# Optimization experiments

Measured on AMD Instinct MI355X. Metric: run time of the kernel, lower is better.

Reference implementation:

```python
import jax, jax.numpy as jnp
import numpy as np

B, S, C, H, D = 4, 1024, 1024, 16, 64
MAX_POS = 512
SPAN = min(max(S, S), MAX_POS)  # rel_attn_span = 512
SCALE = 1.0 / np.sqrt(3.0 * D)


def setup_inputs() -> dict:
    key = jax.random.key(0)
    ks = jax.random.split(key, 10)
    std = 0.02
    return {
        "hidden_states": jax.random.normal(ks[0], (B, S, C), jnp.float32),
        "rel_embeddings": jax.random.normal(ks[1], (2 * MAX_POS, C), jnp.float32),
        "Wq": jax.random.normal(ks[2], (C, H, D), jnp.float32) * std,
        "bq": jnp.zeros((H, D), jnp.float32),
        "Wk": jax.random.normal(ks[3], (C, H, D), jnp.float32) * std,
        "Wv": jax.random.normal(ks[4], (C, H, D), jnp.float32) * std,
        "bv": jnp.zeros((H, D), jnp.float32),
        "Wc2p": jax.random.normal(ks[5], (C, H, D), jnp.float32) * std,
        "Wp2c": jax.random.normal(ks[6], (C, H, D), jnp.float32) * std,
        "bp2c": jnp.zeros((H, D), jnp.float32),
        "Wo": jax.random.normal(ks[7], (C, C), jnp.float32) * std,
        "bo": jnp.zeros((C,), jnp.float32),
    }


def reference(hidden_states, rel_embeddings, Wq, bq, Wk, Wv, bv, Wc2p, Wp2c, bp2c, Wo, bo):
    # Projections: 'abc,cde->abde'  -> [B,S,H,D]
    q = jnp.einsum("bsc,chd->bshd", hidden_states, Wq) + bq
    k = jnp.einsum("bsc,chd->bshd", hidden_states, Wk)
    v = jnp.einsum("bsc,chd->bshd", hidden_states, Wv) + bv

    q = q * SCALE
    # content-to-content scores: 'aecd,abcd->acbe' -> [B,H,Q,K]
    scores = jnp.einsum("bkhd,bqhd->bhqk", k, q)

    # relative-position ids: rel_pos[q,k] = q - k, shape [S,S]
    ids = jnp.arange(S, dtype=jnp.int32)
    rel_pos = ids[:, None] - ids[None, :]

    # slice rel table to the active span (full table here since S >= MAX_POS)
    rel = rel_embeddings[MAX_POS - SPAN : MAX_POS + SPAN, :]  # [2*SPAN, C]

    # c2p: pos_key [2*SPAN,H,D]; scores [B,H,Q,2*SPAN]; gather along last axis
    pos_key = jnp.einsum("rc,chd->rhd", rel, Wc2p)
    c2p = jnp.einsum("bqhd,rhd->bhqr", q, pos_key)
    c2p_pos = jnp.clip(rel_pos + SPAN, 0, 2 * SPAN - 1)  # [Q,K]
    c2p_idx = jnp.broadcast_to(c2p_pos[None, None], (B, H, S, S))
    c2p_g = jnp.take_along_axis(c2p, c2p_idx, axis=-1)

    # p2c: pos_query (scaled) [2*SPAN,H,D]; scores [B,H,K,2*SPAN]
    pos_query = (jnp.einsum("rc,chd->rhd", rel, Wp2c) + bp2c) * SCALE
    p2c = jnp.einsum("bkhd,rhd->bhkr", k, pos_query)
    p2c_pos = jnp.clip(-rel_pos + SPAN, 0, 2 * SPAN - 1)  # [K,K]
    p2c_idx = jnp.broadcast_to(p2c_pos[None, None], (B, H, S, S))
    p2c_g = jnp.take_along_axis(p2c, p2c_idx, axis=-1)

    scores = scores + c2p_g + p2c_g
    # NOTE: source calls _masked_softmax without passing attention_mask -> plain softmax
    probs = jax.nn.softmax(scores, axis=-1)

    # 'acbe,aecd->abcd' -> [B,Q,H,D]
    attn_out = jnp.einsum("bhqk,bkhd->bqhd", probs, v)
    attn_out = attn_out.reshape(B, S, H * D)
    return jnp.einsum("bsc,cd->bsd", attn_out, Wo) + bo
```

## Files before the change

### kernel.cpp

```cpp
#include <hip/hip_runtime.h>
#include <cmath>

#define SCALE_F 0.07216878364870322f

typedef unsigned short u16;
typedef __attribute__((ext_vector_type(8))) __bf16 bf16x8;
typedef __attribute__((ext_vector_type(4))) float f32x4;
typedef __attribute__((ext_vector_type(16))) float f32x16;

#define MFMA16(a, b, c) __builtin_amdgcn_mfma_f32_16x16x32_bf16(a, b, c, 0, 0, 0)
#define MFMA32(a, b, c) __builtin_amdgcn_mfma_f32_32x32x16_bf16(a, b, c, 0, 0, 0)

__device__ __forceinline__ u16 f2bf(float x) {
    unsigned u = __float_as_uint(x);
    unsigned r = (u + 0x7fffu + ((u >> 16) & 1u)) >> 16;
    return (u16)r;
}
__device__ __forceinline__ float bf2f(u16 u) {
    return __uint_as_float(((unsigned)u) << 16);
}
__device__ __forceinline__ void split2(float x, u16& h, u16& l) {
    h = f2bf(x);
    l = f2bf(x - bf2f(h));
}

__device__ __forceinline__ void glds16(const u16* g, u16* s) {
    __builtin_amdgcn_global_load_lds(
        (const __attribute__((address_space(1))) unsigned int*)g,
        (__attribute__((address_space(3))) unsigned int*)s,
        16, 0, 0);
}

__device__ __forceinline__ bf16x8 frg(const u16* base, int row, int ch) {
    return *(const bf16x8*)(base + (row << 6) + ((ch ^ (row & 7)) << 3));
}

__global__ __launch_bounds__(256) void split_rows2(
    const float* __restrict__ x0, u16* __restrict__ h0, u16* __restrict__ l0,
    int nblk0,
    const float* __restrict__ x1, u16* __restrict__ h1, u16* __restrict__ l1)
{
    const float* x; u16* h; u16* l; int bx = blockIdx.x;
    if (bx < nblk0) { x = x0; h = h0; l = l0; }
    else { x = x1; h = h1; l = l1; bx -= nblk0; }
    int i = (bx * 256 + threadIdx.x) << 2;
    float4 v = *(const float4*)(x + i);
    ushort4 hv, lv;
    split2(v.x, hv.x, lv.x); split2(v.y, hv.y, lv.y);
    split2(v.z, hv.z, lv.z); split2(v.w, hv.w, lv.w);
    *(ushort4*)(h + i) = hv;
    *(ushort4*)(l + i) = lv;
}

__global__ __launch_bounds__(256) void transpose3(
    const float* __restrict__ W0, u16* __restrict__ Th0, u16* __restrict__ Tl0,
    const float* __restrict__ W1, u16* __restrict__ Th1, u16* __restrict__ Tl1,
    const float* __restrict__ W2, u16* __restrict__ Th2, u16* __restrict__ Tl2)
{
    const float* W; u16* Th; u16* Tl;
    if (blockIdx.z == 0)      { W = W0; Th = Th0; Tl = Tl0; }
    else if (blockIdx.z == 1) { W = W1; Th = Th1; Tl = Tl1; }
    else                      { W = W2; Th = Th2; Tl = Tl2; }
    __shared__ float t[64][65];
    const int tid = threadIdx.x;
    const int r = tid >> 4, c4 = (tid & 15) << 2;
    const int k0 = blockIdx.y << 6, n0 = blockIdx.x << 6;
#pragma unroll
    for (int p = 0; p < 4; ++p) {
        int row = (p << 4) + r;
        float4 v = *(const float4*)(W + (size_t)(k0 + row) * 1024 + n0 + c4);
        t[row][c4] = v.x; t[row][c4 + 1] = v.y; t[row][c4 + 2] = v.z; t[row][c4 + 3] = v.w;
    }
    __syncthreads();
#pragma unroll
    for (int p = 0; p < 4; ++p) {
        int nr = (p << 4) + r;
        float a = t[c4 + 0][nr];
        float b = t[c4 + 1][nr];
        float c = t[c4 + 2][nr];
        float d = t[c4 + 3][nr];
        ushort4 hv, lv;
        split2(a, hv.x, lv.x); split2(b, hv.y, lv.y);
        split2(c, hv.z, lv.z); split2(d, hv.w, lv.w);
        *(ushort4*)(Th + (size_t)(n0 + nr) * 1024 + k0 + c4) = hv;
        *(ushort4*)(Tl + (size_t)(n0 + nr) * 1024 + k0 + c4) = lv;
    }
}

struct GD {
    const u16 *Ah, *Al, *Bh, *Bl;
    const float* bias;
    float* Cf;
    u16 *Ch, *Cl;
    int N, K;
    float scale;
    int mode;
};

__global__ __launch_bounds__(256, 2) void gemm_mfma(GD d0, GD d1, int xsplit)
{
    __shared__ u16 sAh[128 * 32];
    __shared__ u16 sAl[128 * 32];
    __shared__ u16 sBh[128 * 32];
    __shared__ u16 sBl[128 * 32];

    const GD d = (blockIdx.x < (unsigned)xsplit) ? d0 : d1;
    const int bx = (blockIdx.x < (unsigned)xsplit) ? blockIdx.x : blockIdx.x - xsplit;
    const int N = d.N, K = d.K;

    const int tid = threadIdx.x;
    const int wv = tid >> 6, lane = tid & 63;
    const int quad = lane >> 4, ln = lane & 15;
    const int wr = wv & 1, wc = wv >> 1;
    const int m0 = blockIdx.y << 7, n0 = bx << 7;

    const u16* gsrc = (wv == 0) ? d.Ah : (wv == 1) ? d.Al : (wv == 2) ? d.Bh : d.Bl;
    u16* sdst = (wv == 0) ? sAh : (wv == 1) ? sAl : (wv == 2) ? sBh : sBl;
    const int row0 = (wv < 2) ? m0 : n0;
    const u16* gbase = gsrc + (size_t)(row0 + (lane >> 2)) * K + ((lane & 3) << 3);

    f32x4 acc[4][4];
#pragma unroll
    for (int f = 0; f < 4; ++f)
#pragma unroll
        for (int g = 0; g < 4; ++g) acc[f][g] = (f32x4){0.f, 0.f, 0.f, 0.f};

    const u16* pa_h = sAh + ((wr << 6) + ln) * 32 + (quad << 3);
    const u16* pa_l = sAl + ((wr << 6) + ln) * 32 + (quad << 3);
    const u16* pb_h = sBh + ((wc << 6) + ln) * 32 + (quad << 3);
    const u16* pb_l = sBl + ((wc << 6) + ln) * 32 + (quad << 3);

#pragma unroll
    for (int t = 0; t < 8; ++t)
        glds16(gbase + (size_t)(t << 4) * K, sdst + t * 512);

    for (int kt = 0; kt < K; kt += 32) {
        __syncthreads();
        bf16x8 bhv[4], blv[4], ahv[4], alv[4];
#pragma unroll
        for (int g = 0; g < 4; ++g) {
            bhv[g] = *(const bf16x8*)(pb_h + g * 512);
            blv[g] = *(const bf16x8*)(pb_l + g * 512);
            ahv[g] = *(const bf16x8*)(pa_h + g * 512);
            alv[g] = *(const bf16x8*)(pa_l + g * 512);
        }
        __syncthreads();
        if (kt + 32 < K) {
#pragma unroll
            for (int t = 0; t < 8; ++t)
                glds16(gbase + (size_t)(t << 4) * K + (kt + 32), sdst + t * 512);
        }
#pragma unroll
        for (int f = 0; f < 4; ++f) {
#pragma unroll
            for (int g = 0; g < 4; ++g) {
                acc[f][g] = MFMA16(ahv[f], bhv[g], acc[f][g]);
                acc[f][g] = MFMA16(ahv[f], blv[g], acc[f][g]);
                acc[f][g] = MFMA16(alv[f], bhv[g], acc[f][g]);
            }
        }
    }

    if (d.mode == 0) {
#pragma unroll
        for (int f = 0; f < 4; ++f) {
            int row = m0 + (wr << 6) + (f << 4) + (quad << 2);
#pragma unroll
            for (int g = 0; g < 4; ++g) {
                int col = n0 + (wc << 6) + (g << 4) + ln;
                float bb = d.bias ? d.bias[col] : 0.f;
#pragma unroll
                for (int r = 0; r < 4; ++r)
                    d.Cf[(size_t)(row + r) * N + col] = (acc[f][g][r] + bb) * d.scale;
            }
        }
    } else if (d.mode == 1) {
#pragma unroll
        for (int f = 0; f < 4; ++f) {
            int row = m0 + (wr << 6) + (f << 4) + (quad << 2);
#pragma unroll
            for (int g = 0; g < 4; ++g) {
                int col = n0 + (wc << 6) + (g << 4) + ln;
                float bb = d.bias ? d.bias[col] : 0.f;
#pragma unroll
                for (int r = 0; r < 4; ++r) {
                    float v = (acc[f][g][r] + bb) * d.scale;
                    u16 hh, ll;
                    split2(v, hh, ll);
                    d.Ch[(size_t)(row + r) * N + col] = hh;
                    d.Cl[(size_t)(row + r) * N + col] = ll;
                }
            }
        }
    } else if (d.mode == 2) {
#pragma unroll
        for (int f = 0; f < 4; ++f) {
            int row = m0 + (wr << 6) + (f << 4) + (quad << 2);
#pragma unroll
            for (int g = 0; g < 4; ++g) {
                int col = n0 + (wc << 6) + (g << 4) + ln;
                size_t obase = (size_t)(col >> 10) * 1048576 + (col & 1023);
#pragma unroll
                for (int r = 0; r < 4; ++r) {
                    float v = acc[f][g][r] + (d.bias ? d.bias[row + r] : 0.f);
                    u16 hh, ll;
                    split2(v, hh, ll);
                    size_t idx = obase + (size_t)(row + r) * 1024;
                    d.Ch[idx] = hh;
                    d.Cl[idx] = ll;
                }
            }
        }
    } else {
#pragma unroll
        for (int f = 0; f < 4; ++f) {
            int row = m0 + (wr << 6) + (f << 4) + (quad << 2);
#pragma unroll
            for (int g = 0; g < 4; ++g) {
                int col = n0 + (wc << 6) + (g << 4) + ln;
                float bb = d.bias ? d.bias[col] : 0.f;
#pragma unroll
                for (int r = 0; r < 4; ++r)
                    d.Ch[(size_t)(row + r) * N + col] =
                        f2bf((acc[f][g][r] + bb) * d.scale);
            }
        }
    }
}

__global__ __launch_bounds__(256, 2) void gemm_mfma_64(GD d0, GD d1, int xsplit)
{
    __shared__ u16 sAh[64 * 32];
    __shared__ u16 sAl[64 * 32];
    __shared__ u16 sBh[128 * 32];
    __shared__ u16 sBl[128 * 32];

    const GD d = (blockIdx.x < (unsigned)xsplit) ? d0 : d1;
    const int bx = (blockIdx.x < (unsigned)xsplit) ? blockIdx.x : blockIdx.x - xsplit;
    const int N = d.N, K = d.K;

    const int tid = threadIdx.x;
    const int wv = tid >> 6, lane = tid & 63;
    const int quad = lane >> 4, ln = lane & 15;
    const int wr = wv & 1, wc = wv >> 1;
    const int m0 = blockIdx.y << 6, n0 = bx << 7;

    const u16* gsrc = (wv == 0) ? d.Ah : (wv == 1) ? d.Al : (wv == 2) ? d.Bh : d.Bl;
    u16* sdst = (wv == 0) ? sAh : (wv == 1) ? sAl : (wv == 2) ? sBh : sBl;
    const int row0 = (wv < 2) ? m0 : n0;
    const int nt = (wv < 2) ? 4 : 8;
    const u16* gbase = gsrc + (size_t)(row0 + (lane >> 2)) * K + ((lane & 3) << 3);

    f32x4 acc[2][4];
#pragma unroll
    for (int f = 0; f < 2; ++f)
#pragma unroll
        for (int g = 0; g < 4; ++g) acc[f][g] = (f32x4){0.f, 0.f, 0.f, 0.f};

    const u16* pa_h = sAh + ((wr << 5) + ln) * 32 + (quad << 3);
    const u16* pa_l = sAl + ((wr << 5) + ln) * 32 + (quad << 3);
    const u16* pb_h = sBh + ((wc << 6) + ln) * 32 + (quad << 3);
    const u16* pb_l = sBl + ((wc << 6) + ln) * 32 + (quad << 3);

#pragma unroll
    for (int t = 0; t < 8; ++t)
        if (t < nt) glds16(gbase + (size_t)(t << 4) * K, sdst + t * 512);

    for (int kt = 0; kt < K; kt += 32) {
        __syncthreads();
        bf16x8 bhv[4], blv[4], ahv[2], alv[2];
#pragma unroll
        for (int g = 0; g < 4; ++g) {
            bhv[g] = *(const bf16x8*)(pb_h + g * 512);
            blv[g] = *(const bf16x8*)(pb_l + g * 512);
        }
#pragma unroll
        for (int f = 0; f < 2; ++f) {
            ahv[f] = *(const bf16x8*)(pa_h + f * 512);
            alv[f] = *(const bf16x8*)(pa_l + f * 512);
        }
        __syncthreads();
        if (kt + 32 < K) {
#pragma unroll
            for (int t = 0; t < 8; ++t)
                if (t < nt)
                    glds16(gbase + (size_t)(t << 4) * K + (kt + 32), sdst + t * 512);
        }
#pragma unroll
        for (int f = 0; f < 2; ++f) {
#pragma unroll
            for (int g = 0; g < 4; ++g) {
                acc[f][g] = MFMA16(ahv[f], bhv[g], acc[f][g]);
                acc[f][g] = MFMA16(ahv[f], blv[g], acc[f][g]);
                acc[f][g] = MFMA16(alv[f], bhv[g], acc[f][g]);
            }
        }
    }

    if (d.mode == 0) {
#pragma unroll
        for (int f = 0; f < 2; ++f) {
            int row = m0 + (wr << 5) + (f << 4) + (quad << 2);
#pragma unroll
            for (int g = 0; g < 4; ++g) {
                int col = n0 + (wc << 6) + (g << 4) + ln;
                float bb = d.bias ? d.bias[col] : 0.f;
#pragma unroll
                for (int r = 0; r < 4; ++r)
                    d.Cf[(size_t)(row + r) * N + col] = (acc[f][g][r] + bb) * d.scale;
            }
        }
    } else if (d.mode == 2) {
#pragma unroll
        for (int f = 0; f < 2; ++f) {
            int row = m0 + (wr << 5) + (f << 4) + (quad << 2);
#pragma unroll
            for (int g = 0; g < 4; ++g) {
                int col = n0 + (wc << 6) + (g << 4) + ln;
                size_t obase = (size_t)(col >> 10) * 1048576 + (col & 1023);
#pragma unroll
                for (int r = 0; r < 4; ++r) {
                    float v = acc[f][g][r] + (d.bias ? d.bias[row + r] : 0.f);
                    u16 hh, ll;
                    split2(v, hh, ll);
                    size_t idx = obase + (size_t)(row + r) * 1024;
                    d.Ch[idx] = hh;
                    d.Cl[idx] = ll;
                }
            }
        }
    } else if (d.mode == 3) {
#pragma unroll
        for (int f = 0; f < 2; ++f) {
            int row = m0 + (wr << 5) + (f << 4) + (quad << 2);
#pragma unroll
            for (int g = 0; g < 4; ++g) {
                int col = n0 + (wc << 6) + (g << 4) + ln;
                float bb = d.bias ? d.bias[col] : 0.f;
#pragma unroll
                for (int r = 0; r < 4; ++r)
                    d.Ch[(size_t)(row + r) * N + col] =
                        f2bf((acc[f][g][r] + bb) * d.scale);
            }
        }
    } else {
#pragma unroll
        for (int f = 0; f < 2; ++f) {
            int row = m0 + (wr << 5) + (f << 4) + (quad << 2);
#pragma unroll
            for (int g = 0; g < 4; ++g) {
                int col = n0 + (wc << 6) + (g << 4) + ln;
                float bb = d.bias ? d.bias[col] : 0.f;
#pragma unroll
                for (int r = 0; r < 4; ++r) {
                    float v = (acc[f][g][r] + bb) * d.scale;
                    u16 hh, ll;
                    split2(v, hh, ll);
                    d.Ch[(size_t)(row + r) * N + col] = hh;
                    d.Cl[(size_t)(row + r) * N + col] = ll;
                }
            }
        }
    }
}

__global__ __launch_bounds__(256, 2) void attn_mfma(
    const u16* Qh_g, const u16* Ql_g,
    const u16* __restrict__ Kh_g, const u16* __restrict__ Kl_g,
    const u16* __restrict__ VTh_g, const u16* __restrict__ VTl_g,
    const u16* __restrict__ PKh_g, const u16* __restrict__ PQh_g,
    u16* outh, u16* outl)
{
    __shared__ __align__(16) unsigned char smem[67840];
    u16* Kh_s  = (u16*)smem;
    u16* Kl_s  = (u16*)(smem + 8192);
    u16* PKs   = (u16*)(smem + 16384);
    u16* VTh_s = (u16*)(smem + 16384);
    u16* VTl_s = (u16*)(smem + 24576);
    u16* PQs   = (u16*)(smem + 32768);
    u16* Ph    = (u16*)(smem + 49152);
    u16* Pl    = (u16*)(smem + 58368);
    float* Mbase = (float*)(smem + 49152);
    float* l_s = (float*)(smem + 67584);

    const int tid = threadIdx.x;
    const int wv = tid >> 6, lane = tid & 63;
    const int half = lane >> 5, lc = lane & 31;
    const int rw = wv & 1, cw = wv >> 1;
    const int b = blockIdx.z, h = blockIdx.y;
    const int q0 = blockIdx.x << 6, hd0 = h << 6;
    float* Mw = Mbase + wv * 1056;

    const int rloc = lane >> 3;
    const int k4e  = (((lane & 7) ^ rloc) << 3);

    bf16x8 qfh[4], qfl[4], kfh[4], kfl[4];
    const size_t arow = ((size_t)(b * 1024 + q0 + (rw << 5) + lc) << 10) + hd0 + (half << 3);
    {
#pragma unroll
        for (int c = 0; c < 4; ++c) {
            qfh[c] = *(const bf16x8*)(Qh_g + arow + (c << 4));
            qfl[c] = *(const bf16x8*)(Ql_g + arow + (c << 4));
            kfh[c] = *(const bf16x8*)(Kh_g + arow + (c << 4));
            kfl[c] = *(const bf16x8*)(Kl_g + arow + (c << 4));
        }
    }
    if (tid < 64) l_s[tid] = 0.f;

    f32x16 o;
    float l_part[16];
#pragma unroll
    for (int r = 0; r < 16; ++r) { o[r] = 0.f; l_part[r] = 0.f; }

    const int sbC = (rw - cw + 1) << 5;
    const int sbP = (cw - rw + 1) << 5;

    {
#pragma unroll
        for (int t = 0; t < 2; ++t) {
            int call = wv + (t << 2);
            int row = (call << 3) + rloc;
            size_t g = ((size_t)(b * 1024 + 0 + row) << 10) + hd0 + k4e;
            glds16(Kh_g + g, Kh_s + (call << 9));
            glds16(Kl_g + g, Kl_s + (call << 9));
        }
        const int baseC = q0 + 449, baseP = -q0 + 449;
#pragma unroll
        for (int t = 0; t < 4; ++t) {
            int call = wv + (t << 2);
            int row = (call << 3) + rloc;
            int rc = min(max(baseC + row, 0), 1023);
            int rp = min(max(baseP + row, 0), 1023);
            glds16(PKh_g + (((size_t)rc << 10) + hd0 + k4e), PKs + (call << 9));
            glds16(PQh_g + (((size_t)rp << 10) + hd0 + k4e), PQs + (call << 9));
        }
    }
    __syncthreads();

    for (int kt = 0; kt < 16; ++kt) {
        const int k0 = kt << 6;
        f32x16 s;
#pragma unroll
        for (int r = 0; r < 16; ++r) s[r] = 0.f;
        {
            const int krow = (cw << 5) + lc;
#pragma unroll
            for (int c = 0; c < 4; ++c) {
                int ch = (c << 1) + half;
                bf16x8 bh = frg(Kh_s, krow, ch);
                bf16x8 bl = frg(Kl_s, krow, ch);
                s = MFMA32(qfh[c], bh, s);
                s = MFMA32(qfh[c], bl, s);
                s = MFMA32(qfl[c], bh, s);
            }
        }
        {
            f32x16 M0, M1;
#pragma unroll
            for (int r = 0; r < 16; ++r) { M0[r] = 0.f; M1[r] = 0.f; }
#pragma unroll
            for (int c = 0; c < 4; ++c) {
                int ch = (c << 1) + half;
                bf16x8 b0 = frg(PKs, sbC + lc, ch);
                bf16x8 b1 = frg(PKs, sbC + 32 + lc, ch);
                M0 = MFMA32(qfh[c], b0, M0); M0 = MFMA32(qfl[c], b0, M0);
                M1 = MFMA32(qfh[c], b1, M1); M1 = MFMA32(qfl[c], b1, M1);
            }
#pragma unroll
            for (int r = 0; r < 16; ++r) {
                int m = (r & 3) + ((r >> 2) << 3) + (half << 2);
                bool u = (lc >= m);
                float val = u ? M0[r] : M1[r];
                int nn = m - lc + (u ? 31 : -1);
                Mw[m * 33 + nn] = val;
            }
#pragma unroll
            for (int r = 0; r < 16; ++r) {
                int m = (r & 3) + ((r >> 2) << 3) + (half << 2);
                s[r] += Mw[m * 33 + lc];
            }
        }
        {
            f32x16 M0, M1;
#pragma unroll
            for (int r = 0; r < 16; ++r) { M0[r] = 0.f; M1[r] = 0.f; }
#pragma unroll
            for (int c = 0; c < 4; ++c) {
                int ch = (c << 1) + half;
                bf16x8 b0 = frg(PQs, sbP + lc, ch);
                bf16x8 b1 = frg(PQs, sbP + 32 + lc, ch);
                M0 = MFMA32(kfh[c], b0, M0); M0 = MFMA32(kfl[c], b0, M0);
                M1 = MFMA32(kfh[c], b1, M1); M1 = MFMA32(kfl[c], b1, M1);
            }
#pragma unroll
            for (int r = 0; r < 16; ++r) {
                int m = (r & 3) + ((r >> 2) << 3) + (half << 2);
                bool u = (lc >= 31 - m);
                float val = u ? M0[r] : M1[r];
                int nn = lc + m + (u ? -31 : 1);
                Mw[m * 33 + nn] = val;
            }
#pragma unroll
            for (int r = 0; r < 16; ++r) {
                int m = (r & 3) + ((r >> 2) << 3) + (half << 2);
                s[r] += Mw[m * 33 + lc];
            }
        }
#pragma unroll
        for (int r = 0; r < 16; ++r) {
            s[r] = __expf(s[r]);
            l_part[r] += s[r];
        }
        __syncthreads();
        {
#pragma unroll
            for (int t = 0; t < 2; ++t) {
                int call = wv + (t << 2);
                int row = (call << 3) + rloc;
                size_t g = ((size_t)((b * 16 + h) * 64 + row) << 10) + k0 + k4e;
                glds16(VTh_g + g, VTh_s + (call << 9));
                glds16(VTl_g + g, VTl_s + (call << 9));
            }
        }
#pragma unroll
        for (int r = 0; r < 16; ++r) {
            int m = (r & 3) + ((r >> 2) << 3) + (half << 2);
            int addr = ((rw << 5) + m) * 72 + (cw << 5) + lc;
            u16 hh, ll;
            split2(s[r], hh, ll);
            Ph[addr] = hh;
            Pl[addr] = ll;
        }
        __syncthreads();
        {
            const u16* ap  = Ph + ((rw << 5) + lc) * 72 + (half << 3);
            const u16* apl = Pl + ((rw << 5) + lc) * 72 + (half << 3);
            const int vrow = (cw << 5) + lc;
#pragma unroll
            for (int c = 0; c < 4; ++c) {
                int ch = (c << 1) + half;
                bf16x8 ah = *(const bf16x8*)(ap + (c << 4));
                bf16x8 al = *(const bf16x8*)(apl + (c << 4));
                bf16x8 bh = frg(VTh_s, vrow, ch);
                bf16x8 bl = frg(VTl_s, vrow, ch);
                o = MFMA32(ah, bh, o);
                o = MFMA32(ah, bl, o);
                o = MFMA32(al, bh, o);
            }
        }
        __syncthreads();
        {
            const int k0n = ((kt + 1) & 15) << 6;
#pragma unroll
            for (int t = 0; t < 2; ++t) {
                int call = wv + (t << 2);
                int row = (call << 3) + rloc;
                size_t g = ((size_t)(b * 1024 + k0n + row) << 10) + hd0 + k4e;
                glds16(Kh_g + g, Kh_s + (call << 9));
                glds16(Kl_g + g, Kl_s + (call << 9));
            }
            const int baseC = q0 - k0n + 449, baseP = k0n - q0 + 449;
#pragma unroll
            for (int t = 0; t < 4; ++t) {
                int call = wv + (t << 2);
                int row = (call << 3) + rloc;
                int rc = min(max(baseC + row, 0), 1023);
                int rp = min(max(baseP + row, 0), 1023);
                glds16(PKh_g + (((size_t)rc << 10) + hd0 + k4e), PKs + (call << 9));
                glds16(PQh_g + (((size_t)rp << 10) + hd0 + k4e), PQs + (call << 9));
            }
        }
        __syncthreads();
    }
#pragma unroll
    for (int r = 0; r < 16; ++r) {
        float v = l_part[r];
#pragma unroll
        for (int off = 1; off < 32; off <<= 1) v += __shfl_xor(v, off, 64);
        int m = (r & 3) + ((r >> 2) << 3) + (half << 2);
        if (lc == 0) atomicAdd(&l_s[(rw << 5) + m], v);
    }
    __syncthreads();
#pragma unroll
    for (int r = 0; r < 16; ++r) {
        int m = (r & 3) + ((r >> 2) << 3) + (half << 2);
        int row = (rw << 5) + m;
        float inv = 1.f / l_s[row];
        size_t g = ((size_t)(b * 1024 + q0 + row) << 10) + hd0 + (cw << 5) + lc;
        u16 hh, ll;
        split2(o[r] * inv, hh, ll);
        outh[g] = hh;
        outl[g] = ll;
    }
}

extern "C" void kernel_launch(void* const* d_in, const int* in_sizes, int n_in,
                              void* d_out, int out_size, void* d_ws, size_t ws_size,
                              hipStream_t stream)
{
    (void)in_sizes; (void)n_in; (void)out_size; (void)ws_size;
    const float* hidden = (const float*)d_in[0];
    const float* rel    = (const float*)d_in[1];
    const float* Wq   = (const float*)d_in[2];
    const float* bq   = (const float*)d_in[3];
    const float* Wk   = (const float*)d_in[4];
    const float* Wv   = (const float*)d_in[5];
    const float* bv   = (const float*)d_in[6];
    const float* Wc2p = (const float*)d_in[7];
    const float* Wp2c = (const float*)d_in[8];
    const float* bp2c = (const float*)d_in[9];
    const float* Wo   = (const float*)d_in[10];
    const float* bo   = (const float*)d_in[11];
    float* out = (float*)d_out;

    u16* U = (u16*)d_ws;
    const size_t MU = 1048576;
    u16* Hh  = U;              u16* Hl  = U + 4 * MU;
    u16* Rh  = U + 8 * MU;     u16* Rl  = U + 9 * MU;
    u16* WtAh = U + 10 * MU;   u16* WtAl = U + 11 * MU;
    u16* Qh  = U + 12 * MU;    u16* Ql  = U + 16 * MU;
    u16* Kh  = U + 20 * MU;    u16* Kl  = U + 24 * MU;
    u16* VTh = U + 28 * MU;    u16* VTl = U + 32 * MU;
    u16* WkTh = U + 28 * MU;   u16* WkTl = U + 29 * MU;
    u16* PKh = U + 0 * MU;
    u16* PQh = U + 2 * MU;
    u16* Wp2cTh = U + 4 * MU;  u16* Wp2cTl = U + 5 * MU;
    u16* WoTh = U + 6 * MU;    u16* WoTl = U + 7 * MU;

    dim3 blk(256);

    hipLaunchKernelGGL(split_rows2, dim3(5120), blk, 0, stream,
                       hidden, Hh, Hl, 4096, rel, Rh, Rl);

    hipLaunchKernelGGL(transpose3, dim3(16, 16, 2), blk, 0, stream,
                       Wq, WtAh, WtAl, Wk, WkTh, WkTl,
                       (const float*)nullptr, (u16*)nullptr, (u16*)nullptr);

    {
        GD dQ = {Hh, Hl, WtAh, WtAl, bq, nullptr, Qh, Ql, 1024, 1024, SCALE_F, 1};
        GD dK = {Hh, Hl, WkTh, WkTl, nullptr, nullptr, Kh, Kl, 1024, 1024, 1.f, 1};
        hipLaunchKernelGGL(gemm_mfma, dim3(16, 32), blk, 0, stream, dQ, dK, 8);
    }

    hipLaunchKernelGGL(transpose3, dim3(16, 16, 1), blk, 0, stream,
                       Wv, WtAh, WtAl,
                       (const float*)nullptr, (u16*)nullptr, (u16*)nullptr,
                       (const float*)nullptr, (u16*)nullptr, (u16*)nullptr);

    {
        GD dV = {WtAh, WtAl, Hh, Hl, bv, nullptr, VTh, VTl, 4096, 1024, 1.f, 2};
        hipLaunchKernelGGL(gemm_mfma_64, dim3(32, 16), blk, 0, stream, dV, dV, 9999);
    }

    hipLaunchKernelGGL(transpose3, dim3(16, 16, 3), blk, 0, stream,
                       Wc2p, WtAh, WtAl, Wp2c, Wp2cTh, Wp2cTl, Wo, WoTh, WoTl);

    {
        GD dPK = {Rh, Rl, WtAh, WtAl, nullptr, nullptr, PKh, nullptr, 1024, 1024, 1.f, 3};
        GD dPQ = {Rh, Rl, Wp2cTh, Wp2cTl, bp2c, nullptr, PQh, nullptr, 1024, 1024, SCALE_F, 3};
        hipLaunchKernelGGL(gemm_mfma_64, dim3(16, 16), blk, 0, stream, dPK, dPQ, 8);
    }

    hipLaunchKernelGGL(attn_mfma, dim3(16, 16, 4), blk, 0, stream,
                       Qh, Ql, Kh, Kl, VTh, VTl, PKh, PQh, Qh, Ql);

    {
        GD dO = {Qh, Ql, WoTh, WoTl, bo, out, nullptr, nullptr, 1024, 1024, 1.f, 0};
        hipLaunchKernelGGL(gemm_mfma_64, dim3(8, 64), blk, 0, stream, dO, dO, 9999);
    }
}
```

Before: 468.0 us.

## Double-buffer GEMM LDS tiles and restructure attention loop to overlap V loads

Both GEMM kernels now hold two LDS stages. The load for the next K-tile is issued right after the barrier into the alternate buffer, which removes one of the two barriers per iteration. In the attention kernel, V^T and P get their own LDS regions, so the V^T tile load starts at the top of each KV iteration and overlaps the score computation. The P·V MFMAs are moved after the next K/PK/PQ prefetch, and the P buffer uses an XOR-swizzled layout read through the same fragment helper. This doubles LDS per block (GEMM 64KB, attention 80KB), which can lower occupancy relative to the launch_bounds(256,2) target.

```diff
diff --git a/kernel.cpp b/kernel.cpp
--- a/kernel.cpp
+++ b/kernel.cpp
@@ -99,10 +99,10 @@
 
 __global__ __launch_bounds__(256, 2) void gemm_mfma(GD d0, GD d1, int xsplit)
 {
-    __shared__ u16 sAh[128 * 32];
-    __shared__ u16 sAl[128 * 32];
-    __shared__ u16 sBh[128 * 32];
-    __shared__ u16 sBl[128 * 32];
+    __shared__ u16 sAh[8192];
+    __shared__ u16 sAl[8192];
+    __shared__ u16 sBh[8192];
+    __shared__ u16 sBl[8192];
 
     const GD d = (blockIdx.x < (unsigned)xsplit) ? d0 : d1;
     const int bx = (blockIdx.x < (unsigned)xsplit) ? blockIdx.x : blockIdx.x - xsplit;
@@ -134,21 +134,23 @@
     for (int t = 0; t < 8; ++t)
         glds16(gbase + (size_t)(t << 4) * K, sdst + t * 512);
 
+    int cur = 0;
     for (int kt = 0; kt < K; kt += 32) {
         __syncthreads();
+        if (kt + 32 < K) {
+            u16* nd = sdst + ((cur ^ 1) << 12);
+#pragma unroll
+            for (int t = 0; t < 8; ++t)
+                glds16(gbase + (size_t)(t << 4) * K + (kt + 32), nd + t * 512);
+        }
+        const int co = cur << 12;
         bf16x8 bhv[4], blv[4], ahv[4], alv[4];
 #pragma unroll
         for (int g = 0; g < 4; ++g) {
-            bhv[g] = *(const bf16x8*)(pb_h + g * 512);
-            blv[g] = *(const bf16x8*)(pb_l + g * 512);
-            ahv[g] = *(const bf16x8*)(pa_h + g * 512);
-            alv[g] = *(const bf16x8*)(pa_l + g * 512);
-        }
-        __syncthreads();
-        if (kt + 32 < K) {
-#pragma unroll
-            for (int t = 0; t < 8; ++t)
-                glds16(gbase + (size_t)(t << 4) * K + (kt + 32), sdst + t * 512);
+            bhv[g] = *(const bf16x8*)(pb_h + co + g * 512);
+            blv[g] = *(const bf16x8*)(pb_l + co + g * 512);
+            ahv[g] = *(const bf16x8*)(pa_h + co + g * 512);
+            alv[g] = *(const bf16x8*)(pa_l + co + g * 512);
         }
 #pragma unroll
         for (int f = 0; f < 4; ++f) {
@@ -159,6 +161,7 @@
                 acc[f][g] = MFMA16(alv[f], bhv[g], acc[f][g]);
             }
         }
+        cur ^= 1;
     }
 
     if (d.mode == 0) {
@@ -230,10 +233,10 @@
 
 __global__ __launch_bounds__(256, 2) void gemm_mfma_64(GD d0, GD d1, int xsplit)
 {
-    __shared__ u16 sAh[64 * 32];
-    __shared__ u16 sAl[64 * 32];
-    __shared__ u16 sBh[128 * 32];
-    __shared__ u16 sBl[128 * 32];
+    __shared__ u16 sAh[4096];
+    __shared__ u16 sAl[4096];
+    __shared__ u16 sBh[8192];
+    __shared__ u16 sBl[8192];
 
     const GD d = (blockIdx.x < (unsigned)xsplit) ? d0 : d1;
     const int bx = (blockIdx.x < (unsigned)xsplit) ? blockIdx.x : blockIdx.x - xsplit;
@@ -249,6 +252,7 @@
     u16* sdst = (wv == 0) ? sAh : (wv == 1) ? sAl : (wv == 2) ? sBh : sBl;
     const int row0 = (wv < 2) ? m0 : n0;
     const int nt = (wv < 2) ? 4 : 8;
+    const int sw = (wv < 2) ? 2048 : 4096;
     const u16* gbase = gsrc + (size_t)(row0 + (lane >> 2)) * K + ((lane & 3) << 3);
 
     f32x4 acc[2][4];
@@ -266,25 +270,27 @@
     for (int t = 0; t < 8; ++t)
         if (t < nt) glds16(gbase + (size_t)(t << 4) * K, sdst + t * 512);
 
+    int cur = 0;
     for (int kt = 0; kt < K; kt += 32) {
         __syncthreads();
-        bf16x8 bhv[4], blv[4], ahv[2], alv[2];
-#pragma unroll
-        for (int g = 0; g < 4; ++g) {
-            bhv[g] = *(const bf16x8*)(pb_h + g * 512);
-            blv[g] = *(const bf16x8*)(pb_l + g * 512);
-        }
-#pragma unroll
-        for (int f = 0; f < 2; ++f) {
-            ahv[f] = *(const bf16x8*)(pa_h + f * 512);
-            alv[f] = *(const bf16x8*)(pa_l + f * 512);
-        }
-        __syncthreads();
         if (kt + 32 < K) {
+            u16* nd = sdst + (cur ^ 1) * sw;
 #pragma unroll
             for (int t = 0; t < 8; ++t)
                 if (t < nt)
-                    glds16(gbase + (size_t)(t << 4) * K + (kt + 32), sdst + t * 512);
+                    glds16(gbase + (size_t)(t << 4) * K + (kt + 32), nd + t * 512);
+        }
+        const int ca = cur << 11, cb = cur << 12;
+        bf16x8 bhv[4], blv[4], ahv[2], alv[2];
+#pragma unroll
+        for (int g = 0; g < 4; ++g) {
+            bhv[g] = *(const bf16x8*)(pb_h + cb + g * 512);
+            blv[g] = *(const bf16x8*)(pb_l + cb + g * 512);
+        }
+#pragma unroll
+        for (int f = 0; f < 2; ++f) {
+            ahv[f] = *(const bf16x8*)(pa_h + ca + f * 512);
+            alv[f] = *(const bf16x8*)(pa_l + ca + f * 512);
         }
 #pragma unroll
         for (int f = 0; f < 2; ++f) {
@@ -295,6 +301,7 @@
                 acc[f][g] = MFMA16(alv[f], bhv[g], acc[f][g]);
             }
         }
+        cur ^= 1;
     }
 
     if (d.mode == 0) {
@@ -371,17 +378,17 @@
     const u16* __restrict__ PKh_g, const u16* __restrict__ PQh_g,
     u16* outh, u16* outl)
 {
-    __shared__ __align__(16) unsigned char smem[67840];
+    __shared__ __align__(16) unsigned char smem[81920];
     u16* Kh_s  = (u16*)smem;
     u16* Kl_s  = (u16*)(smem + 8192);
     u16* PKs   = (u16*)(smem + 16384);
-    u16* VTh_s = (u16*)(smem + 16384);
-    u16* VTl_s = (u16*)(smem + 24576);
     u16* PQs   = (u16*)(smem + 32768);
-    u16* Ph    = (u16*)(smem + 49152);
-    u16* Pl    = (u16*)(smem + 58368);
-    float* Mbase = (float*)(smem + 49152);
-    float* l_s = (float*)(smem + 67584);
+    u16* VTh_s = (u16*)(smem + 49152);
+    u16* VTl_s = (u16*)(smem + 57344);
+    u16* Ph    = (u16*)(smem + 65536);
+    u16* Pl    = (u16*)(smem + 73728);
+    float* Mbase = (float*)(smem + 65536);
+    float* l_s = (float*)smem;
 
     const int tid = threadIdx.x;
     const int wv = tid >> 6, lane = tid & 63;
@@ -389,7 +396,8 @@
     const int rw = wv & 1, cw = wv >> 1;
     const int b = blockIdx.z, h = blockIdx.y;
     const int q0 = blockIdx.x << 6, hd0 = h << 6;
-    float* Mw = Mbase + wv * 1056;
+    float* Mw = Mbase + (wv << 10);
+    const int h4 = half << 2;
 
     const int rloc = lane >> 3;
     const int k4e  = (((lane & 7) ^ rloc) << 3);
@@ -405,7 +413,6 @@
             kfl[c] = *(const bf16x8*)(Kl_g + arow + (c << 4));
         }
     }
-    if (tid < 64) l_s[tid] = 0.f;
 
     f32x16 o;
     float l_part[16];
@@ -420,7 +427,7 @@
         for (int t = 0; t < 2; ++t) {
             int call = wv + (t << 2);
             int row = (call << 3) + rloc;
-            size_t g = ((size_t)(b * 1024 + 0 + row) << 10) + hd0 + k4e;
+            size_t g = ((size_t)(b * 1024 + row) << 10) + hd0 + k4e;
             glds16(Kh_g + g, Kh_s + (call << 9));
             glds16(Kl_g + g, Kl_s + (call << 9));
         }
@@ -439,6 +446,16 @@
 
     for (int kt = 0; kt < 16; ++kt) {
         const int k0 = kt << 6;
+        {
+#pragma unroll
+            for (int t = 0; t < 2; ++t) {
+                int call = wv + (t << 2);
+                int row = (call << 3) + rloc;
+                size_t g = ((size_t)((b * 16 + h) * 64 + row) << 10) + k0 + k4e;
+                glds16(VTh_g + g, VTh_s + (call << 9));
+                glds16(VTl_g + g, VTl_s + (call << 9));
+            }
+        }
         f32x16 s;
 #pragma unroll
         for (int r = 0; r < 16; ++r) s[r] = 0.f;
@@ -468,16 +485,16 @@
             }
 #pragma unroll
             for (int r = 0; r < 16; ++r) {
-                int m = (r & 3) + ((r >> 2) << 3) + (half << 2);
+                int m = (r & 3) + ((r >> 2) << 3) + h4;
                 bool u = (lc >= m);
                 float val = u ? M0[r] : M1[r];
                 int nn = m - lc + (u ? 31 : -1);
-                Mw[m * 33 + nn] = val;
+                Mw[(m << 5) + nn] = val;
             }
 #pragma unroll
             for (int r = 0; r < 16; ++r) {
-                int m = (r & 3) + ((r >> 2) << 3) + (half << 2);
-                s[r] += Mw[m * 33 + lc];
+                int m = (r & 3) + ((r >> 2) << 3) + h4;
+                s[r] += Mw[(m << 5) + lc];
             }
         }
         {
@@ -494,16 +511,16 @@
             }
 #pragma unroll
             for (int r = 0; r < 16; ++r) {
-                int m = (r & 3) + ((r >> 2) << 3) + (half << 2);
+                int m = (r & 3) + ((r >> 2) << 3) + h4;
                 bool u = (lc >= 31 - m);
                 float val = u ? M0[r] : M1[r];
                 int nn = lc + m + (u ? -31 : 1);
-                Mw[m * 33 + nn] = val;
+                Mw[(m << 5) + nn] = val;
             }
 #pragma unroll
             for (int r = 0; r < 16; ++r) {
-                int m = (r & 3) + ((r >> 2) << 3) + (half << 2);
-                s[r] += Mw[m * 33 + lc];
+                int m = (r & 3) + ((r >> 2) << 3) + h4;
+                s[r] += Mw[(m << 5) + lc];
             }
         }
 #pragma unroll
@@ -513,39 +530,17 @@
         }
         __syncthreads();
         {
-#pragma unroll
-            for (int t = 0; t < 2; ++t) {
-                int call = wv + (t << 2);
-                int row = (call << 3) + rloc;
-                size_t g = ((size_t)((b * 16 + h) * 64 + row) << 10) + k0 + k4e;
-                glds16(VTh_g + g, VTh_s + (call << 9));
-                glds16(VTl_g + g, VTl_s + (call << 9));
-            }
-        }
-#pragma unroll
-        for (int r = 0; r < 16; ++r) {
-            int m = (r & 3) + ((r >> 2) << 3) + (half << 2);
-            int addr = ((rw << 5) + m) * 72 + (cw << 5) + lc;
-            u16 hh, ll;
-            split2(s[r], hh, ll);
-            Ph[addr] = hh;
-            Pl[addr] = ll;
-        }
-        __syncthreads();
-        {
-            const u16* ap  = Ph + ((rw << 5) + lc) * 72 + (half << 3);
-            const u16* apl = Pl + ((rw << 5) + lc) * 72 + (half << 3);
-            const int vrow = (cw << 5) + lc;
-#pragma unroll
-            for (int c = 0; c < 4; ++c) {
-                int ch = (c << 1) + half;
-                bf16x8 ah = *(const bf16x8*)(ap + (c << 4));
-                bf16x8 al = *(const bf16x8*)(apl + (c << 4));
-                bf16x8 bh = frg(VTh_s, vrow, ch);
-                bf16x8 bl = frg(VTl_s, vrow, ch);
-                o = MFMA32(ah, bh, o);
-                o = MFMA32(ah, bl, o);
-                o = MFMA32(al, bh, o);
+            const int cx3 = ((((cw << 2) + (lc >> 3)) ^ h4) << 3);
+            const int cole = lc & 7;
+            const int rb = (rw << 5) + h4;
+#pragma unroll
+            for (int r = 0; r < 16; ++r) {
+                const int m_lo = (r & 3) + ((r >> 2) << 3);
+                u16 hh, ll;
+                split2(s[r], hh, ll);
+                int addr = ((rb + m_lo) << 6) + ((cx3 ^ ((r & 3) << 3)) | cole);
+                Ph[addr] = hh;
+                Pl[addr] = ll;
             }
         }
         __syncthreads();
@@ -570,21 +565,41 @@
                 glds16(PQh_g + (((size_t)rp << 10) + hd0 + k4e), PQs + (call << 9));
             }
         }
+        {
+            const int prow = (rw << 5) + lc;
+            const int vrow = (cw << 5) + lc;
+#pragma unroll
+            for (int c = 0; c < 4; ++c) {
+                int ch = (c << 1) + half;
+                bf16x8 ah = frg(Ph, prow, ch);
+                bf16x8 al = frg(Pl, prow, ch);
+                bf16x8 bh = frg(VTh_s, vrow, ch);
+                bf16x8 bl = frg(VTl_s, vrow, ch);
+                o = MFMA32(ah, bh, o);
+                o = MFMA32(ah, bl, o);
+                o = MFMA32(al, bh, o);
+            }
+        }
         __syncthreads();
     }
+
+    if (tid < 64) l_s[tid] = 0.f;
+    __syncthreads();
 #pragma unroll
     for (int r = 0; r < 16; ++r) {
         float v = l_part[r];
 #pragma unroll
         for (int off = 1; off < 32; off <<= 1) v += __shfl_xor(v, off, 64);
-        int m = (r & 3) + ((r >> 2) << 3) + (half << 2);
-        if (lc == 0) atomicAdd(&l_s[(rw << 5) + m], v);
+        if (lc == 0) {
+            const int m_lo = (r & 3) + ((r >> 2) << 3);
+            atomicAdd(&l_s[(rw << 5) + m_lo + h4], v);
+        }
     }
     __syncthreads();
 #pragma unroll
     for (int r = 0; r < 16; ++r) {
-        int m = (r & 3) + ((r >> 2) << 3) + (half << 2);
-        int row = (rw << 5) + m;
+        const int m_lo = (r & 3) + ((r >> 2) << 3);
+        int row = (rw << 5) + m_lo + h4;
         float inv = 1.f / l_s[row];
         size_t g = ((size_t)(b * 1024 + q0 + row) << 10) + hd0 + (cw << 5) + lc;
         u16 hh, ll;
```

After: 588.8 us. 25.8% more time.
